# Optimization experiments

Hardware: AMD Instinct MI355X
Metric: run time of the kernel (lower is better)

## Reference

```python
import jax, jax.numpy as jnp
import numpy as np

HIDDEN = 4096
NUM_EXPERTS = 64
TOP_K = 8
N_TOKENS = 16384


def setup_inputs() -> dict:
    key = jax.random.key(0)
    kx, kw, kb = jax.random.split(key, 3)
    x = jax.random.normal(kx, (N_TOKENS, HIDDEN), dtype=jnp.float32)
    # nn.Linear(hidden, num_experts): weight [E, H], bias [E]
    bound = 1.0 / np.sqrt(HIDDEN)
    gate_w = jax.random.uniform(kw, (NUM_EXPERTS, HIDDEN), dtype=jnp.float32, minval=-bound, maxval=bound)
    gate_b = jax.random.uniform(kb, (NUM_EXPERTS,), dtype=jnp.float32, minval=-bound, maxval=bound)
    return {"x": x, "gate_w": gate_w, "gate_b": gate_b}


def reference(x, gate_w, gate_b):
    # gate linear: [N, H] @ [H, E] + [E] -> [N, E]
    router_logits = jnp.einsum('nh,eh->ne', x, gate_w) + gate_b
    router_prob = jax.nn.softmax(router_logits, axis=1)
    # top-k over experts
    router_weights, expert_indices = jax.lax.top_k(router_prob, TOP_K)  # [N, K]
    router_weights = router_weights / jnp.sum(router_weights, axis=-1, keepdims=True)
    router_weights = router_weights.astype(x.dtype)
    # one-hot expert mask [N, K, E] -> permute(2,1,0) -> [E, K, N]
    expert_mask = jax.nn.one_hot(expert_indices, NUM_EXPERTS, dtype=jnp.int32)
    expert_mask = jnp.transpose(expert_mask, (2, 1, 0))
    return (router_logits, router_weights, expert_indices, expert_mask)
```

## Files before the change

kernel.cpp:

```cpp
#include <hip/hip_runtime.h>
#include <math.h>

#define NT   16384
#define HD   4096
#define NE   64
#define TOPK 8

#define L_OFF 0
#define W_OFF (NT * NE)
#define I_OFF (W_OFF + NT * TOPK)
#define M_OFF (I_OFF + NT * TOPK)

#define BK  64
#define XS_STRIDE 66
#define WS_STRIDE 68

typedef __attribute__((ext_vector_type(4))) float f4;

__global__ __launch_bounds__(256) void kz_mask(f4* __restrict__ p, int n4) {
  f4 z = {0.f, 0.f, 0.f, 0.f};
  for (int i = blockIdx.x * 256 + threadIdx.x; i < n4; i += gridDim.x * 256) p[i] = z;
}

__global__ __launch_bounds__(256, 4) void k_gemm(const float* __restrict__ x,
                                                 const float* __restrict__ w,
                                                 const float* __restrict__ bias,
                                                 float* __restrict__ out) {
  __shared__ float xs[32 * XS_STRIDE];
  __shared__ float ws[64 * WS_STRIDE];

  const int tid  = threadIdx.x;
  const int lane = tid & 63;
  const int wv   = tid >> 6;
  const int wt   = wv >> 1;
  const int we   = wv & 1;
  const int tg   = lane >> 3;
  const int eg   = lane & 7;
  const int tok0 = blockIdx.x * 32;

  f4 acc[2][4];
#pragma unroll
  for (int i = 0; i < 2; ++i)
#pragma unroll
    for (int s = 0; s < 4; ++s) acc[i][s] = (f4){0.f, 0.f, 0.f, 0.f};

  const int sr = tid >> 4;
  const int su = tid & 15;

  f4 xr0 = *(const f4*)(x + (size_t)(tok0 + sr) * HD + su * 4);
  f4 xr1 = *(const f4*)(x + (size_t)(tok0 + 16 + sr) * HD + su * 4);
  f4 wr[4];
#pragma unroll
  for (int p = 0; p < 4; ++p)
    wr[p] = *(const f4*)(w + (size_t)(sr + 16 * p) * HD + su * 4);

  for (int c = 0; c < HD / BK; ++c) {
    __syncthreads();

    *(f4*)(xs + sr * XS_STRIDE + su * 4)        = xr0;
    *(f4*)(xs + (16 + sr) * XS_STRIDE + su * 4) = xr1;
#pragma unroll
    for (int p = 0; p < 4; ++p)
      *(f4*)(ws + (sr + 16 * p) * WS_STRIDE + su * 4) = wr[p];

    if (c + 1 < HD / BK) {
      const int kc = (c + 1) * BK;
      xr0 = *(const f4*)(x + (size_t)(tok0 + sr) * HD + kc + su * 4);
      xr1 = *(const f4*)(x + (size_t)(tok0 + 16 + sr) * HD + kc + su * 4);
#pragma unroll
      for (int p = 0; p < 4; ++p)
        wr[p] = *(const f4*)(w + (size_t)(sr + 16 * p) * HD + kc + su * 4);
    }

    __syncthreads();

#pragma unroll
    for (int st = 0; st < 16; ++st) {
      const int k0 = st * 4;
      f4 xv0 = *(const f4*)(xs + (wt * 16 + tg * 2 + 0) * XS_STRIDE + k0);
      f4 xv1 = *(const f4*)(xs + (wt * 16 + tg * 2 + 1) * XS_STRIDE + k0);
      f4 wf[4];
#pragma unroll
      for (int s = 0; s < 4; ++s)
        wf[s] = *(const f4*)(ws + (we * 32 + eg + 8 * s) * WS_STRIDE + k0);
#pragma unroll
      for (int s = 0; s < 4; ++s) {
#pragma unroll
        for (int j = 0; j < 4; ++j) {
          acc[0][s][j] = fmaf(xv0[j], wf[s][j], acc[0][s][j]);
          acc[1][s][j] = fmaf(xv1[j], wf[s][j], acc[1][s][j]);
        }
      }
    }
  }

#pragma unroll
  for (int i = 0; i < 2; ++i) {
    const int row = tok0 + wt * 16 + tg * 2 + i;
#pragma unroll
    for (int s = 0; s < 4; ++s) {
      const int e = we * 32 + eg + 8 * s;
      float v = acc[i][s][0] + acc[i][s][1] + acc[i][s][2] + acc[i][s][3] + bias[e];
      out[L_OFF + (size_t)row * NE + e] = v;
    }
  }
}

__global__ __launch_bounds__(256) void k_topk(float* __restrict__ out) {
  const int lane = threadIdx.x & 63;
  const int wv   = threadIdx.x >> 6;
  const int t    = blockIdx.x * 4 + wv;

  float v = out[L_OFF + (size_t)t * NE + lane];

  int rank = 0;
  for (int e = 0; e < NE; ++e) {
    float ve = __shfl(v, e);
    rank += (ve > v) || (ve == v && e < lane);
  }

  float m0 = v;
#pragma unroll
  for (int o = 32; o; o >>= 1) m0 = fmaxf(m0, __shfl_xor(m0, o));
  float ev = (rank < TOPK) ? expf(v - m0) : 0.f;
  float s = ev;
#pragma unroll
  for (int o = 32; o; o >>= 1) s += __shfl_xor(s, o);

  if (rank < TOPK) {
    out[W_OFF + (size_t)t * TOPK + rank] = ev / s;
    out[I_OFF + (size_t)t * TOPK + rank] = (float)lane;
    out[M_OFF + ((size_t)lane * TOPK + rank) * NT + t] = 1.0f;
  }
}

extern "C" void kernel_launch(void* const* d_in, const int* in_sizes, int n_in,
                              void* d_out, int out_size, void* d_ws, size_t ws_size,
                              hipStream_t stream) {
  const float* x  = (const float*)d_in[0];
  const float* gw = (const float*)d_in[1];
  const float* gb = (const float*)d_in[2];
  float* out = (float*)d_out;

  kz_mask<<<2048, 256, 0, stream>>>((f4*)(out + M_OFF), (NE * TOPK * NT) / 4);
  k_gemm <<<NT / 32, 256, 0, stream>>>(x, gw, gb, out);
  k_topk <<<NT / 4, 256, 0, stream>>>(out);
}
```

Before: 212.0 us.

## Double-buffer gate GEMM shared tiles with two register prefetch sets

The gate GEMM now keeps two LDS buffers for the x and weight tiles. It also holds two register sets of prefetched global loads, so the next chunk is written to shared memory while the current one is being computed. This leaves one barrier per K-chunk instead of two, and global-load latency can overlap with the FMA loop. In exchange, LDS per block doubles and the launch-bounds occupancy hint drops from 4 to 2 blocks, which may reduce latency hiding from concurrent waves.

```diff
diff --git a/kernel.cpp b/kernel.cpp
--- a/kernel.cpp
+++ b/kernel.cpp
@@ -22,12 +22,12 @@
   for (int i = blockIdx.x * 256 + threadIdx.x; i < n4; i += gridDim.x * 256) p[i] = z;
 }
 
-__global__ __launch_bounds__(256, 4) void k_gemm(const float* __restrict__ x,
+__global__ __launch_bounds__(256, 2) void k_gemm(const float* __restrict__ x,
                                                  const float* __restrict__ w,
                                                  const float* __restrict__ bias,
                                                  float* __restrict__ out) {
-  __shared__ float xs[32 * XS_STRIDE];
-  __shared__ float ws[64 * WS_STRIDE];
+  __shared__ float xs[2][32 * XS_STRIDE];
+  __shared__ float ws[2][64 * WS_STRIDE];
 
   const int tid  = threadIdx.x;
   const int lane = tid & 63;
@@ -47,52 +47,80 @@
   const int sr = tid >> 4;
   const int su = tid & 15;
 
-  f4 xr0 = *(const f4*)(x + (size_t)(tok0 + sr) * HD + su * 4);
-  f4 xr1 = *(const f4*)(x + (size_t)(tok0 + 16 + sr) * HD + su * 4);
-  f4 wr[4];
-#pragma unroll
-  for (int p = 0; p < 4; ++p)
-    wr[p] = *(const f4*)(w + (size_t)(sr + 16 * p) * HD + su * 4);
+  const float* xb0 = x + (size_t)(tok0 + sr) * HD + su * 4;
+  const float* xb1 = x + (size_t)(tok0 + 16 + sr) * HD + su * 4;
+  const float* wb0 = w + (size_t)(sr +  0) * HD + su * 4;
+  const float* wb1 = w + (size_t)(sr + 16) * HD + su * 4;
+  const float* wb2 = w + (size_t)(sr + 32) * HD + su * 4;
+  const float* wb3 = w + (size_t)(sr + 48) * HD + su * 4;
 
-  for (int c = 0; c < HD / BK; ++c) {
+#define LOADSET(X0, X1, W0, W1, W2, W3, c)            \
+  do { const int kc_ = (c) * BK;                      \
+    X0 = *(const f4*)(xb0 + kc_);                     \
+    X1 = *(const f4*)(xb1 + kc_);                     \
+    W0 = *(const f4*)(wb0 + kc_);                     \
+    W1 = *(const f4*)(wb1 + kc_);                     \
+    W2 = *(const f4*)(wb2 + kc_);                     \
+    W3 = *(const f4*)(wb3 + kc_);                     \
+  } while (0)
+
+#define WRITESET(b, X0, X1, W0, W1, W2, W3)                    \
+  do {                                                         \
+    *(f4*)(&xs[b][sr * XS_STRIDE + su * 4])        = X0;       \
+    *(f4*)(&xs[b][(16 + sr) * XS_STRIDE + su * 4]) = X1;       \
+    *(f4*)(&ws[b][(sr +  0) * WS_STRIDE + su * 4]) = W0;       \
+    *(f4*)(&ws[b][(sr + 16) * WS_STRIDE + su * 4]) = W1;       \
+    *(f4*)(&ws[b][(sr + 32) * WS_STRIDE + su * 4]) = W2;       \
+    *(f4*)(&ws[b][(sr + 48) * WS_STRIDE + su * 4]) = W3;       \
+  } while (0)
+
+#define COMPUTE(b)                                                         \
+  do {                                                                     \
+    _Pragma("unroll")                                                      \
+    for (int st = 0; st < 16; ++st) {                                      \
+      const int k0 = st * 4;                                               \
+      f4 xv0 = *(const f4*)(&xs[b][(wt * 16 + tg * 2 + 0) * XS_STRIDE + k0]); \
+      f4 xv1 = *(const f4*)(&xs[b][(wt * 16 + tg * 2 + 1) * XS_STRIDE + k0]); \
+      f4 wf0 = *(const f4*)(&ws[b][(we * 32 + eg +  0) * WS_STRIDE + k0]); \
+      f4 wf1 = *(const f4*)(&ws[b][(we * 32 + eg +  8) * WS_STRIDE + k0]); \
+      f4 wf2 = *(const f4*)(&ws[b][(we * 32 + eg + 16) * WS_STRIDE + k0]); \
+      f4 wf3 = *(const f4*)(&ws[b][(we * 32 + eg + 24) * WS_STRIDE + k0]); \
+      _Pragma("unroll")                                                    \
+      for (int j = 0; j < 4; ++j) {                                        \
+        acc[0][0][j] = fmaf(xv0[j], wf0[j], acc[0][0][j]);                 \
+        acc[1][0][j] = fmaf(xv1[j], wf0[j], acc[1][0][j]);                 \
+        acc[0][1][j] = fmaf(xv0[j], wf1[j], acc[0][1][j]);                 \
+        acc[1][1][j] = fmaf(xv1[j], wf1[j], acc[1][1][j]);                 \
+        acc[0][2][j] = fmaf(xv0[j], wf2[j], acc[0][2][j]);                 \
+        acc[1][2][j] = fmaf(xv1[j], wf2[j], acc[1][2][j]);                 \
+        acc[0][3][j] = fmaf(xv0[j], wf3[j], acc[0][3][j]);                 \
+        acc[1][3][j] = fmaf(xv1[j], wf3[j], acc[1][3][j]);                 \
+      }                                                                    \
+    }                                                                      \
+  } while (0)
+
+  f4 xA0, xA1, wA0, wA1, wA2, wA3;
+  f4 xB0, xB1, wB0, wB1, wB2, wB3;
+
+  LOADSET(xA0, xA1, wA0, wA1, wA2, wA3, 0);
+  LOADSET(xB0, xB1, wB0, wB1, wB2, wB3, 1);
+  WRITESET(0, xA0, xA1, wA0, wA1, wA2, wA3);
+  __syncthreads();
+
+  for (int cc = 0; cc < 62; cc += 2) {
+    WRITESET(1, xB0, xB1, wB0, wB1, wB2, wB3);
+    LOADSET(xA0, xA1, wA0, wA1, wA2, wA3, cc + 2);
+    COMPUTE(0);
     __syncthreads();
-
-    *(f4*)(xs + sr * XS_STRIDE + su * 4)        = xr0;
-    *(f4*)(xs + (16 + sr) * XS_STRIDE + su * 4) = xr1;
-#pragma unroll
-    for (int p = 0; p < 4; ++p)
-      *(f4*)(ws + (sr + 16 * p) * WS_STRIDE + su * 4) = wr[p];
-
-    if (c + 1 < HD / BK) {
-      const int kc = (c + 1) * BK;
-      xr0 = *(const f4*)(x + (size_t)(tok0 + sr) * HD + kc + su * 4);
-      xr1 = *(const f4*)(x + (size_t)(tok0 + 16 + sr) * HD + kc + su * 4);
-#pragma unroll
-      for (int p = 0; p < 4; ++p)
-        wr[p] = *(const f4*)(w + (size_t)(sr + 16 * p) * HD + kc + su * 4);
-    }
-
+    WRITESET(0, xA0, xA1, wA0, wA1, wA2, wA3);
+    LOADSET(xB0, xB1, wB0, wB1, wB2, wB3, cc + 3);
+    COMPUTE(1);
     __syncthreads();
-
-#pragma unroll
-    for (int st = 0; st < 16; ++st) {
-      const int k0 = st * 4;
-      f4 xv0 = *(const f4*)(xs + (wt * 16 + tg * 2 + 0) * XS_STRIDE + k0);
-      f4 xv1 = *(const f4*)(xs + (wt * 16 + tg * 2 + 1) * XS_STRIDE + k0);
-      f4 wf[4];
-#pragma unroll
-      for (int s = 0; s < 4; ++s)
-        wf[s] = *(const f4*)(ws + (we * 32 + eg + 8 * s) * WS_STRIDE + k0);
-#pragma unroll
-      for (int s = 0; s < 4; ++s) {
-#pragma unroll
-        for (int j = 0; j < 4; ++j) {
-          acc[0][s][j] = fmaf(xv0[j], wf[s][j], acc[0][s][j]);
-          acc[1][s][j] = fmaf(xv1[j], wf[s][j], acc[1][s][j]);
-        }
-      }
-    }
   }
+  WRITESET(1, xB0, xB1, wB0, wB1, wB2, wB3);
+  COMPUTE(0);
+  __syncthreads();
+  COMPUTE(1);
 
 #pragma unroll
   for (int i = 0; i < 2; ++i) {
@@ -104,6 +132,9 @@
       out[L_OFF + (size_t)row * NE + e] = v;
     }
   }
+#undef LOADSET
+#undef WRITESET
+#undef COMPUTE
 }
 
 __global__ __launch_bounds__(256) void k_topk(float* __restrict__ out) {
```

Result: faster. 186.4 us (-12.1%).
